# Optimization experiments

Hardware: AMD Instinct MI355X
Metric: run time of the kernel (lower is better)

Reference implementation:

```python
import jax, jax.numpy as jnp
import numpy as np

KS = 3           # kernel size (conv1, conv2, deform conv)
PAD = 1          # k//2 padding for the dense convs and deform zero-padding
DIM = 256
B, H, W = 4, 64, 64
N = KS * KS      # number of sampling points per output pixel


def conv2d(x, w, b=None, pad=PAD, stride=1):
    out = jax.lax.conv_general_dilated(
        x, w, (stride, stride), [(pad, pad), (pad, pad)],
        dimension_numbers=('NCHW', 'OIHW', 'NCHW'))
    if b is not None:
        out = out + b[None, :, None, None]
    return out


def deform_conv(x, p_w, p_b, dw):
    # DeformConv2d (deform-conv-v2 style, modulation=False)
    b, c, h, w = x.shape
    offset = conv2d(x, p_w, p_b, pad=1)                     # (b, 2N, h, w)
    xp = jnp.pad(x, ((0, 0), (0, 0), (PAD, PAD), (PAD, PAD)))
    Hp, Wp = h + 2 * PAD, w + 2 * PAD

    # kernel-relative offsets p_n: rows first, then cols (row-major flatten)
    r = jnp.arange(-(KS - 1) // 2, (KS - 1) // 2 + 1, dtype=x.dtype)
    pnx, pny = jnp.meshgrid(r, r, indexing='ij')
    p_n = jnp.concatenate([pnx.ravel(), pny.ravel()])       # (2N,)

    # base grid p_0 starts at 1 (consistent with zero padding of 1)
    gy, gx = jnp.meshgrid(jnp.arange(1, h + 1, dtype=x.dtype),
                          jnp.arange(1, w + 1, dtype=x.dtype), indexing='ij')
    p0 = jnp.concatenate([jnp.tile(gy[..., None], (1, 1, N)),
                          jnp.tile(gx[..., None], (1, 1, N))], axis=-1)  # (h,w,2N)

    p = jnp.transpose(offset, (0, 2, 3, 1)) + p_n + p0      # (b,h,w,2N)
    px, py = p[..., :N], p[..., N:]
    fx, fy = jnp.floor(px), jnp.floor(py)
    qlx = jnp.clip(fx, 0, Hp - 1)
    qly = jnp.clip(fy, 0, Wp - 1)
    qrx = jnp.clip(fx + 1, 0, Hp - 1)
    qry = jnp.clip(fy + 1, 0, Wp - 1)
    px = jnp.clip(px, 0, Hp - 1)
    py = jnp.clip(py, 0, Wp - 1)

    # bilinear weights
    g_lt = (1 + qlx - px) * (1 + qly - py)
    g_rb = (1 - qrx + px) * (1 - qry + py)
    g_lb = (1 + qlx - px) * (1 - qry + py)
    g_rt = (1 - qrx + px) * (1 + qly - py)

    xf = xp.reshape(b, c, Hp * Wp)

    def gather(qx, qy):
        idx = (qx.astype(jnp.int32) * Wp + qy.astype(jnp.int32)).reshape(b, -1)
        return jax.vmap(lambda xb, ib: xb[:, ib])(xf, idx).reshape(b, c, h, w, N)

    x_off = (g_lt[:, None] * gather(qlx, qly) + g_rb[:, None] * gather(qrx, qry)
           + g_lb[:, None] * gather(qlx, qry) + g_rt[:, None] * gather(qrx, qly))

    # (b,c,h,w,N) -> (b,c,h*ks,w*ks): kernel row expands h, kernel col expands w
    x_off = x_off.reshape(b, c, h, w, KS, KS).transpose(0, 1, 2, 4, 3, 5)
    x_off = x_off.reshape(b, c, h * KS, w * KS)
    return conv2d(x_off, dw, None, pad=0, stride=KS)       # (b, c, h, w)


def setup_inputs() -> dict:
    key = jax.random.key(0)
    ks = jax.random.split(key, 8)
    s = 1.0 / np.sqrt(DIM * KS * KS)
    return {
        'x':   jax.random.normal(ks[0], (B, DIM, H, W), jnp.float32),
        'w1':  jax.random.normal(ks[1], (DIM, DIM, KS, KS), jnp.float32) * s,
        'b1':  jax.random.normal(ks[2], (DIM,), jnp.float32) * 0.01,
        'w2':  jax.random.normal(ks[3], (DIM, DIM, KS, KS), jnp.float32) * s,
        'b2':  jax.random.normal(ks[4], (DIM,), jnp.float32) * 0.01,
        'p_w': jax.random.normal(ks[5], (2 * N, DIM, 3, 3), jnp.float32) * (0.05 * s),
        'p_b': jnp.zeros((2 * N,), jnp.float32),
        'dw':  jax.random.normal(ks[6], (DIM, DIM, KS, KS), jnp.float32) * s,
    }


def reference(x, w1, b1, w2, b2, p_w, p_b, dw):
    res = jax.nn.relu(conv2d(x, w1, b1, pad=PAD))   # conv1 + ReLU
    res = res + x                                   # residual 1
    res = conv2d(res, w2, b2, pad=PAD)              # conv2
    res = deform_conv(res, p_w, p_b, dw)            # deformable conv
    return res + x                                  # residual 2
```

## Files before the change

### kernel.cpp

```cpp
#include <hip/hip_runtime.h>

#define HW 64
#define NB 4
#define CH 256

typedef __attribute__((address_space(1))) const void* gptr_t;
typedef __attribute__((address_space(3))) void* lptr_t;
typedef __attribute__((ext_vector_type(8))) short bf8v;
typedef __attribute__((ext_vector_type(4))) float f32x4;

__device__ __forceinline__ void gll16(const void* g, void* l) {
  __builtin_amdgcn_global_load_lds((gptr_t)g, (lptr_t)l, 16, 0, 0);
}
__device__ __forceinline__ ushort f2b(float f) {
  union { float f; uint u; } v; v.f = f;
  uint r = v.u + 0x7FFF + ((v.u >> 16) & 1);
  return (ushort)(r >> 16);
}
__device__ __forceinline__ uint cvt_pk_bf16(float lo, float hi) {
  uint r;
  asm("v_cvt_pk_bf16_f32 %0, %1, %2" : "=v"(r) : "v"(lo), "v"(hi));
  return r;
}
__device__ __forceinline__ float asf(uint u) {
  union { uint u; float f; } v; v.u = u; return v.f;
}

__device__ __forceinline__ void combine_store(
    const uint4& c0, const uint4& c1, const uint4& c2, const uint4& c3,
    const float4& gw, ushort* dst)
{
  uint o[4];
  const uint* p0 = (const uint*)&c0; const uint* p1 = (const uint*)&c1;
  const uint* p2 = (const uint*)&c2; const uint* p3 = (const uint*)&c3;
  #pragma unroll
  for (int w = 0; w < 4; ++w) {
    const float lo = gw.x * asf(p0[w] << 16) + gw.y * asf(p1[w] << 16)
                   + gw.z * asf(p2[w] << 16) + gw.w * asf(p3[w] << 16);
    const float hi = gw.x * asf(p0[w] & 0xffff0000u) + gw.y * asf(p1[w] & 0xffff0000u)
                   + gw.z * asf(p2[w] & 0xffff0000u) + gw.w * asf(p3[w] & 0xffff0000u);
    o[w] = cvt_pk_bf16(lo, hi);
  }
  uint4 r; r.x = o[0]; r.y = o[1]; r.z = o[2]; r.w = o[3];
  *(uint4*)dst = r;
}

__global__ __launch_bounds__(256) void zero_borders_k(
    ushort* __restrict__ xpad, ushort* __restrict__ res1, ushort* __restrict__ res2)
{
  const int buf = blockIdx.x >> 2, b = blockIdx.x & 3;
  ushort* base = (buf == 0 ? xpad : buf == 1 ? res1 : res2) + (size_t)b * 4356 * 256;
  uint4 z; z.x = 0; z.y = 0; z.z = 0; z.w = 0;
  for (int u = threadIdx.x; u < 260 * 32; u += 256) {
    const int p = u >> 5, k = u & 31;
    int r, cc;
    if (p < 66)       { r = 0;       cc = p; }
    else if (p < 132) { r = 65;      cc = p - 66; }
    else if (p < 196) { r = p - 131; cc = 0; }
    else              { r = p - 195; cc = 65; }
    *(uint4*)&base[((size_t)r * 66 + cc) * 256 + k * 8] = z;
  }
}

__global__ __launch_bounds__(256) void pack_x_k(
    const float* __restrict__ x, ushort* __restrict__ xpad)
{
  __shared__ float tile[64][261];
  const int t = threadIdx.x, b = blockIdx.x >> 6, i = blockIdx.x & 63;
  const int wave = t >> 6, l = t & 63;
  const float* src = x + (size_t)b * CH * 4096 + (size_t)i * 64;
  for (int cc = 0; cc < 64; ++cc) {
    const int c = cc * 4 + wave;
    tile[l][c] = src[(size_t)c * 4096 + l];
  }
  __syncthreads();
  const int c0 = (t & 31) * 8;
  #pragma unroll
  for (int jj = 0; jj < 8; ++jj) {
    const int j = (t >> 5) + jj * 8;
    const float4 v0 = *(const float4*)&tile[j][c0];
    const float4 v1 = *(const float4*)&tile[j][c0 + 4];
    uint4 o;
    o.x = cvt_pk_bf16(v0.x, v0.y);
    o.y = cvt_pk_bf16(v0.z, v0.w);
    o.z = cvt_pk_bf16(v1.x, v1.y);
    o.w = cvt_pk_bf16(v1.z, v1.w);
    *(uint4*)&xpad[((size_t)b * 4356 + (i + 1) * 66 + (j + 1)) * 256 + c0] = o;
  }
}

__global__ __launch_bounds__(256) void pack_w_k(
    const float* __restrict__ w1, const float* __restrict__ w2,
    const float* __restrict__ dw, const float* __restrict__ pw,
    const float* __restrict__ pb,
    ushort* __restrict__ wpk1, ushort* __restrict__ wpk2,
    ushort* __restrict__ dwpk, ushort* __restrict__ wpkO, float* __restrict__ pbias)
{
  const int id = blockIdx.x * 256 + threadIdx.x;
  if (id < 3 * 73728) {
    const int tsel = id / 73728, r = id % 73728;
    const int kc = r & 3, o = (r >> 2) & 255, ct = r >> 10;
    const int cb = ct / 9, tap = ct % 9;
    const float* w = (tsel == 0) ? w1 : (tsel == 1) ? w2 : dw;
    const float* s = w + ((size_t)o * CH + cb * 32 + kc * 8) * 9 + tap;
    ushort* d = ((tsel == 0) ? wpk1 : (tsel == 1) ? wpk2 : dwpk) + (size_t)r * 8;
    #pragma unroll
    for (int j = 0; j < 8; ++j) d[j] = f2b(s[j * 9]);
  } else if (id < 3 * 73728 + 9216) {
    const int r = id - 3 * 73728;
    const int kc = r & 3, o = (r >> 2) & 31, ct = r >> 7;
    const int cb = ct / 9, tap = ct % 9;
    ushort* d = wpkO + (size_t)r * 8;
    if (o < 18) {
      const float* s = pw + ((size_t)o * CH + cb * 32 + kc * 8) * 9 + tap;
      #pragma unroll
      for (int j = 0; j < 8; ++j) d[j] = f2b(s[j * 9]);
    } else {
      #pragma unroll
      for (int j = 0; j < 8; ++j) d[j] = 0;
    }
  }
  if (id < 32) pbias[id] = (id < 18) ? pb[id] : 0.f;
}

template<int OTOT, int OUTMODE>
__global__ __launch_bounds__(256, 4) void conv_mfma(
    const ushort* __restrict__ apad, const ushort* __restrict__ wpk,
    const float* __restrict__ bias, const float* __restrict__ xres,
    void* __restrict__ outp)
{
  __shared__ __align__(16) ushort patch[2][6336];
  const int t = threadIdx.x, wave = t >> 6, l = t & 63;
  const int ot  = (OTOT == 256) ? (blockIdx.x >> 8) : 0;
  const int rem = blockIdx.x & 255;
  const int b = rem >> 6, i = rem & 63;
  const int ln = l & 15, kc8 = (l >> 4) * 8;

  constexpr int FO = (OTOT == 256) ? 1 : 2;
  constexpr int FP = (OTOT == 256) ? 4 : 1;
  const int oS  = (OTOT == 256) ? (ot * 64 + wave * 16) : 0;
  const int pxB = (OTOT == 256) ? 0 : (wave * 16);

  const ushort* rowbase = apad + ((size_t)(b * 66 + i) * 66) * 256;

  f32x4 acc[FO][FP];
  #pragma unroll
  for (int a = 0; a < FO; ++a)
    #pragma unroll
    for (int d = 0; d < FP; ++d) acc[a][d] = (f32x4){0.f, 0.f, 0.f, 0.f};

  #define STAGE(buf, cb)                                                        \
    _Pragma("unroll")                                                           \
    for (int it = 0; it < 4; ++it) {                                            \
      const int e = t + it * 256;                                               \
      if (it < 3 || t < 24) {                                                   \
        const int r = e / 264, u = e - r * 264;                                 \
        const int p = r * 66 + (u >> 2);                                        \
        const int sl = (u & 3) ^ ((p >> 1) & 3);                                \
        const ushort* s = rowbase + (size_t)p * 256 + (cb) * 32 + sl * 8;       \
        gll16(s, (ushort*)&patch[buf][0] + (size_t)e * 8);                      \
      }                                                                         \
    }

  STAGE(0, 0)
  for (int cb = 0; cb < 8; ++cb) {
    __syncthreads();
    bf8v wfr[9][FO];
    #pragma unroll
    for (int tap = 0; tap < 9; ++tap)
      #pragma unroll
      for (int fo = 0; fo < FO; ++fo)
        wfr[tap][fo] = *(const bf8v*)&wpk[((size_t)((cb * 9 + tap) * OTOT) + oS + fo * 16 + ln) * 32 + kc8];
    if (cb < 7) { STAGE((cb + 1) & 1, cb + 1) }
    const ushort* pbuf = &patch[cb & 1][0];
    __builtin_amdgcn_s_setprio(1);
    #pragma unroll
    for (int tap = 0; tap < 9; ++tap) {
      const int ky = tap / 3, kx = tap % 3;
      bf8v pf[FP];
      #pragma unroll
      for (int fp = 0; fp < FP; ++fp) {
        const int px = pxB + fp * 16 + ln;
        const int pix = ky * 66 + px + kx;
        const int sl = (l >> 4) ^ ((pix >> 1) & 3);
        pf[fp] = *(const bf8v*)&pbuf[pix * 32 + sl * 8];
      }
      #pragma unroll
      for (int fo = 0; fo < FO; ++fo)
        #pragma unroll
        for (int fp = 0; fp < FP; ++fp)
          acc[fo][fp] = __builtin_amdgcn_mfma_f32_16x16x32_bf16(wfr[tap][fo], pf[fp], acc[fo][fp], 0, 0, 0);
    }
    __builtin_amdgcn_s_setprio(0);
  }
  #undef STAGE

  #pragma unroll
  for (int fo = 0; fo < FO; ++fo) {
    #pragma unroll
    for (int fp = 0; fp < FP; ++fp) {
      const f32x4 a = acc[fo][fp];
      const int o = oS + fo * 16 + (l >> 4) * 4;
      const int j = pxB + fp * 16 + ln;
      const float4 bv = *(const float4*)&bias[o];
      float v0 = a[0] + bv.x, v1 = a[1] + bv.y, v2 = a[2] + bv.z, v3 = a[3] + bv.w;
      if (OUTMODE == 0) {
        const size_t xb = (((size_t)b * CH + o) * HW + i) * HW + j;
        v0 = fmaxf(v0, 0.f) + xres[xb];
        v1 = fmaxf(v1, 0.f) + xres[xb + 4096];
        v2 = fmaxf(v2, 0.f) + xres[xb + 8192];
        v3 = fmaxf(v3, 0.f) + xres[xb + 12288];
      }
      if (OUTMODE == 2) {
        float* op = (float*)outp + ((size_t)b * 4096 + i * 64 + j) * 32 + o;
        float4 r; r.x = v0; r.y = v1; r.z = v2; r.w = v3;
        *(float4*)op = r;
      } else {
        ushort* op = (ushort*)outp + ((size_t)b * 4356 + (i + 1) * 66 + (j + 1)) * 256 + o;
        ushort4 s; s.x = f2b(v0); s.y = f2b(v1); s.z = f2b(v2); s.w = f2b(v3);
        *(ushort4*)op = s;
      }
    }
  }
}

__global__ __launch_bounds__(512) void deform_mfma(
    const ushort* __restrict__ res2pad, const float* __restrict__ offs,
    const ushort* __restrict__ dwpk, const float* __restrict__ x,
    float* __restrict__ out)
{
  __shared__ __align__(16) ushort samp[18432];
  __shared__ __align__(16) int    tblI[576 * 4];
  __shared__ __align__(16) float  tblW[576 * 4];

  const int t = threadIdx.x, wave = t >> 6, l = t & 63;
  const int ohalf = blockIdx.x >> 8;
  const int idx = blockIdx.x & 255;
  const int blk = (idx & 7) * 32 + (idx >> 3);
  const int b = blk >> 6, i = blk & 63;
  const int ln = l & 15, kc8 = (l >> 4) * 8;
  const int oS = ohalf * 128 + wave * 16;

  #pragma unroll
  for (int k2 = 0; k2 < 2; ++k2) {
    const int e = t + k2 * 512;
    if (e < 576) {
      const int n = e >> 6, j = e & 63;
      const int ki = n / 3, kj = n % 3;
      const float offr = offs[((size_t)(b * 64 + i) * 64 + j) * 32 + n];
      const float offc = offs[((size_t)(b * 64 + i) * 64 + j) * 32 + 9 + n];
      const float prow = offr + (float)(ki - 1) + (float)(i + 1);
      const float pcol = offc + (float)(kj - 1) + (float)(j + 1);
      const float fx = floorf(prow), fy = floorf(pcol);
      const float qlx = fminf(fmaxf(fx, 0.f), 65.f);
      const float qly = fminf(fmaxf(fy, 0.f), 65.f);
      const float qrx = fminf(fmaxf(fx + 1.f, 0.f), 65.f);
      const float qry = fminf(fmaxf(fy + 1.f, 0.f), 65.f);
      const float pr  = fminf(fmaxf(prow, 0.f), 65.f);
      const float pc  = fminf(fmaxf(pcol, 0.f), 65.f);
      tblI[e * 4 + 0] = ((int)qlx * 66 + (int)qly) * 512;
      tblI[e * 4 + 1] = ((int)qrx * 66 + (int)qry) * 512;
      tblI[e * 4 + 2] = ((int)qlx * 66 + (int)qry) * 512;
      tblI[e * 4 + 3] = ((int)qrx * 66 + (int)qly) * 512;
      tblW[e * 4 + 0] = (1.f + qlx - pr) * (1.f + qly - pc);
      tblW[e * 4 + 1] = (1.f - qrx + pr) * (1.f - qry + pc);
      tblW[e * 4 + 2] = (1.f + qlx - pr) * (1.f - qry + pc);
      tblW[e * 4 + 3] = (1.f - qrx + pr) * (1.f + qly - pc);
    }
  }

  f32x4 acc[4];
  #pragma unroll
  for (int a = 0; a < 4; ++a) acc[a] = (f32x4){0.f, 0.f, 0.f, 0.f};

  const char* res2b = (const char*)(res2pad + (size_t)b * 4356 * 256);

  #define SAMPLE_CB(cb_)                                                        \
    _Pragma("unroll")                                                           \
    for (int k = 0; k < 5; ++k) {                                               \
      if (k < 4 || t < 256) {                                                   \
        const int u = t + k * 512;                                              \
        const int e = u >> 2, i16 = u & 3;                                      \
        const int4 iv = *(const int4*)&tblI[e * 4];                             \
        const float4 gw = *(const float4*)&tblW[e * 4];                         \
        const char* gb = res2b + (cb_) * 64 + i16 * 16;                         \
        const uint4 c0 = *(const uint4*)(gb + iv.x);                            \
        const uint4 c1 = *(const uint4*)(gb + iv.y);                            \
        const uint4 c2 = *(const uint4*)(gb + iv.z);                            \
        const uint4 c3 = *(const uint4*)(gb + iv.w);                            \
        const int sl = i16 ^ ((e >> 1) & 3);                                    \
        combine_store(c0, c1, c2, c3, gw, &samp[(size_t)e * 32 + sl * 8]);      \
      }                                                                         \
    }

  __syncthreads();
  SAMPLE_CB(0)
  __syncthreads();

  const int rsl = ((l >> 4) ^ ((ln >> 1) & 3)) * 8;

  for (int cb = 0; cb < 8; ++cb) {
    const ushort* wbase = dwpk + (size_t)(cb * 9) * 256 * 32;

    bf8v bfrA[3], bfrB[3];
    #pragma unroll
    for (int q = 0; q < 3; ++q)
      bfrA[q] = *(const bf8v*)&wbase[((size_t)q * 256 + oS + ln) * 32 + kc8];

    #pragma unroll
    for (int ch = 0; ch < 3; ++ch) {
      if (ch < 2) {
        #pragma unroll
        for (int q = 0; q < 3; ++q)
          bfrB[q] = *(const bf8v*)&wbase[((size_t)((ch + 1) * 3 + q) * 256 + oS + ln) * 32 + kc8];
      }
      __builtin_amdgcn_s_setprio(1);
      #pragma unroll
      for (int q = 0; q < 3; ++q) {
        const int tap = ch * 3 + q;
        #pragma unroll
        for (int fp = 0; fp < 4; ++fp) {
          const bf8v af = *(const bf8v*)&samp[(tap * 64 + fp * 16 + ln) * 32 + rsl];
          acc[fp] = __builtin_amdgcn_mfma_f32_16x16x32_bf16(af, bfrA[q], acc[fp], 0, 0, 0);
        }
      }
      __builtin_amdgcn_s_setprio(0);
      #pragma unroll
      for (int q = 0; q < 3; ++q) bfrA[q] = bfrB[q];
    }

    __syncthreads();
    if (cb < 7) {
      SAMPLE_CB(cb + 1)
      __syncthreads();
    }
  }
  #undef SAMPLE_CB

  #pragma unroll
  for (int fp = 0; fp < 4; ++fp) {
    const f32x4 a = acc[fp];
    const int o = oS + ln;
    const int j0 = fp * 16 + (l >> 4) * 4;
    const size_t base = (((size_t)b * CH + o) * HW + i) * HW + j0;
    const float4 xv = *(const float4*)&x[base];
    float4 r; r.x = a[0] + xv.x; r.y = a[1] + xv.y; r.z = a[2] + xv.z; r.w = a[3] + xv.w;
    *(float4*)&out[base] = r;
  }
}

extern "C" void kernel_launch(void* const* d_in, const int* in_sizes, int n_in,
                              void* d_out, int out_size, void* d_ws, size_t ws_size,
                              hipStream_t stream) {
  (void)in_sizes; (void)n_in; (void)out_size; (void)ws_size;
  const float* x  = (const float*)d_in[0];
  const float* w1 = (const float*)d_in[1];
  const float* b1 = (const float*)d_in[2];
  const float* w2 = (const float*)d_in[3];
  const float* b2 = (const float*)d_in[4];
  const float* pw = (const float*)d_in[5];
  const float* pb = (const float*)d_in[6];
  const float* dw = (const float*)d_in[7];
  float* out = (float*)d_out;

  char* w = (char*)d_ws;
  size_t off = 0;
  auto carve = [&](size_t bytes) { char* p = w + off; off += (bytes + 255) & ~(size_t)255; return p; };
  ushort* xpad  = (ushort*)carve(8929280);
  ushort* res1  = (ushort*)carve(8929280);
  ushort* res2  = (ushort*)carve(8929280);
  ushort* wpk1  = (ushort*)carve(1179648);
  ushort* wpk2  = (ushort*)carve(1179648);
  ushort* wpkO  = (ushort*)carve(147456);
  ushort* dwpk  = (ushort*)carve(1179648);
  float*  pbias = (float*) carve(256);
  float*  offs  = (float*) carve(2097152);

  zero_borders_k<<<12, 256, 0, stream>>>(xpad, res1, res2);
  pack_w_k<<<900, 256, 0, stream>>>(w1, w2, dw, pw, pb, wpk1, wpk2, dwpk, wpkO, pbias);
  pack_x_k<<<256, 256, 0, stream>>>(x, xpad);
  conv_mfma<256, 0><<<1024, 256, 0, stream>>>(xpad, wpk1, b1, x, res1);
  conv_mfma<256, 1><<<1024, 256, 0, stream>>>(res1, wpk2, b2, nullptr, res2);
  conv_mfma<32, 2><<<256, 256, 0, stream>>>(res2, wpkO, pbias, nullptr, offs);
  deform_mfma<<<NB * HW * 2, 512, 0, stream>>>(res2, offs, dwpk, x, out);
}
```

Before: 145.6 us.

## Split deform conv blocks by column half instead of output-channel half

The deform kernel now splits each output row into two 32-column halves across blocks, with 16 waves covering all 256 output channels, instead of splitting output channels in half. Each block therefore samples only its own 32 columns, so the bilinear gather and offset-table work is no longer duplicated across the two channel-half blocks, and shared memory per block is halved. The cost is 1024-thread blocks with fewer MFMA tiles per wave, which may lower latency hiding or occupancy per wave.

```diff
diff --git a/kernel.cpp b/kernel.cpp
--- a/kernel.cpp
+++ b/kernel.cpp
@@ -224,62 +224,59 @@
   }
 }
 
-__global__ __launch_bounds__(512) void deform_mfma(
+__global__ __launch_bounds__(1024) void deform_mfma(
     const ushort* __restrict__ res2pad, const float* __restrict__ offs,
     const ushort* __restrict__ dwpk, const float* __restrict__ x,
     float* __restrict__ out)
 {
-  __shared__ __align__(16) ushort samp[18432];
-  __shared__ __align__(16) int    tblI[576 * 4];
-  __shared__ __align__(16) float  tblW[576 * 4];
+  __shared__ __align__(16) ushort samp[9216];
+  __shared__ __align__(16) int    tblI[288 * 4];
+  __shared__ __align__(16) float  tblW[288 * 4];
 
   const int t = threadIdx.x, wave = t >> 6, l = t & 63;
-  const int ohalf = blockIdx.x >> 8;
+  const int jh = blockIdx.x >> 8;
   const int idx = blockIdx.x & 255;
   const int blk = (idx & 7) * 32 + (idx >> 3);
   const int b = blk >> 6, i = blk & 63;
   const int ln = l & 15, kc8 = (l >> 4) * 8;
-  const int oS = ohalf * 128 + wave * 16;
-
-  #pragma unroll
-  for (int k2 = 0; k2 < 2; ++k2) {
-    const int e = t + k2 * 512;
-    if (e < 576) {
-      const int n = e >> 6, j = e & 63;
-      const int ki = n / 3, kj = n % 3;
-      const float offr = offs[((size_t)(b * 64 + i) * 64 + j) * 32 + n];
-      const float offc = offs[((size_t)(b * 64 + i) * 64 + j) * 32 + 9 + n];
-      const float prow = offr + (float)(ki - 1) + (float)(i + 1);
-      const float pcol = offc + (float)(kj - 1) + (float)(j + 1);
-      const float fx = floorf(prow), fy = floorf(pcol);
-      const float qlx = fminf(fmaxf(fx, 0.f), 65.f);
-      const float qly = fminf(fmaxf(fy, 0.f), 65.f);
-      const float qrx = fminf(fmaxf(fx + 1.f, 0.f), 65.f);
-      const float qry = fminf(fmaxf(fy + 1.f, 0.f), 65.f);
-      const float pr  = fminf(fmaxf(prow, 0.f), 65.f);
-      const float pc  = fminf(fmaxf(pcol, 0.f), 65.f);
-      tblI[e * 4 + 0] = ((int)qlx * 66 + (int)qly) * 512;
-      tblI[e * 4 + 1] = ((int)qrx * 66 + (int)qry) * 512;
-      tblI[e * 4 + 2] = ((int)qlx * 66 + (int)qry) * 512;
-      tblI[e * 4 + 3] = ((int)qrx * 66 + (int)qly) * 512;
-      tblW[e * 4 + 0] = (1.f + qlx - pr) * (1.f + qly - pc);
-      tblW[e * 4 + 1] = (1.f - qrx + pr) * (1.f - qry + pc);
-      tblW[e * 4 + 2] = (1.f + qlx - pr) * (1.f - qry + pc);
-      tblW[e * 4 + 3] = (1.f - qrx + pr) * (1.f + qly - pc);
-    }
-  }
-
-  f32x4 acc[4];
-  #pragma unroll
-  for (int a = 0; a < 4; ++a) acc[a] = (f32x4){0.f, 0.f, 0.f, 0.f};
+  const int oS = wave * 16;
+
+  if (t < 288) {
+    const int n = t >> 5, jj = t & 31;
+    const int j = jh * 32 + jj;
+    const int ki = n / 3, kj = n % 3;
+    const float offr = offs[((size_t)(b * 64 + i) * 64 + j) * 32 + n];
+    const float offc = offs[((size_t)(b * 64 + i) * 64 + j) * 32 + 9 + n];
+    const float prow = offr + (float)(ki - 1) + (float)(i + 1);
+    const float pcol = offc + (float)(kj - 1) + (float)(j + 1);
+    const float fx = floorf(prow), fy = floorf(pcol);
+    const float qlx = fminf(fmaxf(fx, 0.f), 65.f);
+    const float qly = fminf(fmaxf(fy, 0.f), 65.f);
+    const float qrx = fminf(fmaxf(fx + 1.f, 0.f), 65.f);
+    const float qry = fminf(fmaxf(fy + 1.f, 0.f), 65.f);
+    const float pr  = fminf(fmaxf(prow, 0.f), 65.f);
+    const float pc  = fminf(fmaxf(pcol, 0.f), 65.f);
+    tblI[t * 4 + 0] = ((int)qlx * 66 + (int)qly) * 512;
+    tblI[t * 4 + 1] = ((int)qrx * 66 + (int)qry) * 512;
+    tblI[t * 4 + 2] = ((int)qlx * 66 + (int)qry) * 512;
+    tblI[t * 4 + 3] = ((int)qrx * 66 + (int)qly) * 512;
+    tblW[t * 4 + 0] = (1.f + qlx - pr) * (1.f + qly - pc);
+    tblW[t * 4 + 1] = (1.f - qrx + pr) * (1.f - qry + pc);
+    tblW[t * 4 + 2] = (1.f + qlx - pr) * (1.f - qry + pc);
+    tblW[t * 4 + 3] = (1.f - qrx + pr) * (1.f + qly - pc);
+  }
+
+  f32x4 acc[2];
+  acc[0] = (f32x4){0.f, 0.f, 0.f, 0.f};
+  acc[1] = (f32x4){0.f, 0.f, 0.f, 0.f};
 
   const char* res2b = (const char*)(res2pad + (size_t)b * 4356 * 256);
 
   #define SAMPLE_CB(cb_)                                                        \
     _Pragma("unroll")                                                           \
-    for (int k = 0; k < 5; ++k) {                                               \
-      if (k < 4 || t < 256) {                                                   \
-        const int u = t + k * 512;                                              \
+    for (int k = 0; k < 2; ++k) {                                               \
+      if (k == 0 || t < 128) {                                                  \
+        const int u = t + k * 1024;                                             \
         const int e = u >> 2, i16 = u & 3;                                      \
         const int4 iv = *(const int4*)&tblI[e * 4];                             \
         const float4 gw = *(const float4*)&tblW[e * 4];                         \
@@ -319,8 +316,8 @@
       for (int q = 0; q < 3; ++q) {
         const int tap = ch * 3 + q;
         #pragma unroll
-        for (int fp = 0; fp < 4; ++fp) {
-          const bf8v af = *(const bf8v*)&samp[(tap * 64 + fp * 16 + ln) * 32 + rsl];
+        for (int fp = 0; fp < 2; ++fp) {
+          const bf8v af = *(const bf8v*)&samp[(tap * 32 + fp * 16 + ln) * 32 + rsl];
           acc[fp] = __builtin_amdgcn_mfma_f32_16x16x32_bf16(af, bfrA[q], acc[fp], 0, 0, 0);
         }
       }
@@ -338,10 +335,10 @@
   #undef SAMPLE_CB
 
   #pragma unroll
-  for (int fp = 0; fp < 4; ++fp) {
+  for (int fp = 0; fp < 2; ++fp) {
     const f32x4 a = acc[fp];
     const int o = oS + ln;
-    const int j0 = fp * 16 + (l >> 4) * 4;
+    const int j0 = jh * 32 + fp * 16 + (l >> 4) * 4;
     const size_t base = (((size_t)b * CH + o) * HW + i) * HW + j0;
     const float4 xv = *(const float4*)&x[base];
     float4 r; r.x = a[0] + xv.x; r.y = a[1] + xv.y; r.z = a[2] + xv.z; r.w = a[3] + xv.w;
@@ -382,5 +379,5 @@
   conv_mfma<256, 0><<<1024, 256, 0, stream>>>(xpad, wpk1, b1, x, res1);
   conv_mfma<256, 1><<<1024, 256, 0, stream>>>(res1, wpk2, b2, nullptr, res2);
   conv_mfma<32, 2><<<256, 256, 0, stream>>>(res2, wpkO, pbias, nullptr, offs);
-  deform_mfma<<<NB * HW * 2, 512, 0, stream>>>(res2, offs, dwpk, x, out);
-}
+  deform_mfma<<<NB * HW * 2, 1024, 0, stream>>>(res2, offs, dwpk, x, out);
+}
```

Result: slower. 149.2 us (+2.5%).

## Double output channels per block in convs and deform, double-buffer deform samples

Applied to the files above, without the earlier changes.

The dense conv kernels now compute 32 output channels per wave (128 per block) instead of 64 per block, halving the grid and reusing each staged input patch across twice as many channels. Weight fragments are loaded in three chunks of three taps rather than all nine at once, to limit register pressure. The deform kernel now covers all 256 output channels per block, so the bilinear sampling, which was previously done twice for the two channel halves, runs once. Its sample buffer is double-buffered so the next channel block's gather overlaps the MFMAs, with one sync per iteration. The cost is more accumulators per wave, lower occupancy bounds, and only 256 deform blocks and 512 conv blocks, which may underfill the GPU.

```diff
diff --git a/kernel.cpp b/kernel.cpp
--- a/kernel.cpp
+++ b/kernel.cpp
@@ -124,7 +124,7 @@
 }
 
 template<int OTOT, int OUTMODE>
-__global__ __launch_bounds__(256, 4) void conv_mfma(
+__global__ __launch_bounds__(256, 2) void conv_mfma(
     const ushort* __restrict__ apad, const ushort* __restrict__ wpk,
     const float* __restrict__ bias, const float* __restrict__ xres,
     void* __restrict__ outp)
@@ -136,9 +136,9 @@
   const int b = rem >> 6, i = rem & 63;
   const int ln = l & 15, kc8 = (l >> 4) * 8;
 
-  constexpr int FO = (OTOT == 256) ? 1 : 2;
+  constexpr int FO = 2;
   constexpr int FP = (OTOT == 256) ? 4 : 1;
-  const int oS  = (OTOT == 256) ? (ot * 64 + wave * 16) : 0;
+  const int oS  = (OTOT == 256) ? (ot * 128 + wave * 32) : 0;
   const int pxB = (OTOT == 256) ? 0 : (wave * 16);
 
   const ushort* rowbase = apad + ((size_t)(b * 66 + i) * 66) * 256;
@@ -165,33 +165,36 @@
   STAGE(0, 0)
   for (int cb = 0; cb < 8; ++cb) {
     __syncthreads();
-    bf8v wfr[9][FO];
-    #pragma unroll
-    for (int tap = 0; tap < 9; ++tap)
-      #pragma unroll
-      for (int fo = 0; fo < FO; ++fo)
-        wfr[tap][fo] = *(const bf8v*)&wpk[((size_t)((cb * 9 + tap) * OTOT) + oS + fo * 16 + ln) * 32 + kc8];
-    if (cb < 7) { STAGE((cb + 1) & 1, cb + 1) }
     const ushort* pbuf = &patch[cb & 1][0];
-    __builtin_amdgcn_s_setprio(1);
-    #pragma unroll
-    for (int tap = 0; tap < 9; ++tap) {
-      const int ky = tap / 3, kx = tap % 3;
-      bf8v pf[FP];
-      #pragma unroll
-      for (int fp = 0; fp < FP; ++fp) {
-        const int px = pxB + fp * 16 + ln;
-        const int pix = ky * 66 + px + kx;
-        const int sl = (l >> 4) ^ ((pix >> 1) & 3);
-        pf[fp] = *(const bf8v*)&pbuf[pix * 32 + sl * 8];
-      }
-      #pragma unroll
-      for (int fo = 0; fo < FO; ++fo)
+    #pragma unroll
+    for (int ch = 0; ch < 3; ++ch) {
+      bf8v wfr[3][FO];
+      #pragma unroll
+      for (int q = 0; q < 3; ++q) {
+        const int tap = ch * 3 + q;
         #pragma unroll
-        for (int fp = 0; fp < FP; ++fp)
-          acc[fo][fp] = __builtin_amdgcn_mfma_f32_16x16x32_bf16(wfr[tap][fo], pf[fp], acc[fo][fp], 0, 0, 0);
-    }
-    __builtin_amdgcn_s_setprio(0);
+        for (int fo = 0; fo < FO; ++fo)
+          wfr[q][fo] = *(const bf8v*)&wpk[((size_t)((cb * 9 + tap) * OTOT) + oS + fo * 16 + ln) * 32 + kc8];
+      }
+      if (ch == 2 && cb < 7) { STAGE((cb + 1) & 1, cb + 1) }
+      __builtin_amdgcn_s_setprio(1);
+      #pragma unroll
+      for (int q = 0; q < 3; ++q) {
+        const int tap = ch * 3 + q;
+        const int ky = tap / 3, kx = tap % 3;
+        #pragma unroll
+        for (int fp = 0; fp < FP; ++fp) {
+          const int px = pxB + fp * 16 + ln;
+          const int pix = ky * 66 + px + kx;
+          const int sl = (l >> 4) ^ ((pix >> 1) & 3);
+          const bf8v pf = *(const bf8v*)&pbuf[pix * 32 + sl * 8];
+          #pragma unroll
+          for (int fo = 0; fo < FO; ++fo)
+            acc[fo][fp] = __builtin_amdgcn_mfma_f32_16x16x32_bf16(wfr[q][fo], pf, acc[fo][fp], 0, 0, 0);
+        }
+      }
+      __builtin_amdgcn_s_setprio(0);
+    }
   }
   #undef STAGE
 
@@ -224,22 +227,20 @@
   }
 }
 
-__global__ __launch_bounds__(512) void deform_mfma(
+__global__ __launch_bounds__(512, 2) void deform_mfma(
     const ushort* __restrict__ res2pad, const float* __restrict__ offs,
     const ushort* __restrict__ dwpk, const float* __restrict__ x,
     float* __restrict__ out)
 {
-  __shared__ __align__(16) ushort samp[18432];
+  __shared__ __align__(16) ushort samp[2][18432];
   __shared__ __align__(16) int    tblI[576 * 4];
   __shared__ __align__(16) float  tblW[576 * 4];
 
   const int t = threadIdx.x, wave = t >> 6, l = t & 63;
-  const int ohalf = blockIdx.x >> 8;
-  const int idx = blockIdx.x & 255;
-  const int blk = (idx & 7) * 32 + (idx >> 3);
+  const int blk = (blockIdx.x & 7) * 32 + (blockIdx.x >> 3);
   const int b = blk >> 6, i = blk & 63;
   const int ln = l & 15, kc8 = (l >> 4) * 8;
-  const int oS = ohalf * 128 + wave * 16;
+  const int oS = wave * 32;
 
   #pragma unroll
   for (int k2 = 0; k2 < 2; ++k2) {
@@ -269,13 +270,15 @@
     }
   }
 
-  f32x4 acc[4];
-  #pragma unroll
-  for (int a = 0; a < 4; ++a) acc[a] = (f32x4){0.f, 0.f, 0.f, 0.f};
+  f32x4 acc[2][4];
+  #pragma unroll
+  for (int a = 0; a < 2; ++a)
+    #pragma unroll
+    for (int d = 0; d < 4; ++d) acc[a][d] = (f32x4){0.f, 0.f, 0.f, 0.f};
 
   const char* res2b = (const char*)(res2pad + (size_t)b * 4356 * 256);
 
-  #define SAMPLE_CB(cb_)                                                        \
+  #define SAMPLE_CB(cb_, buf_)                                                  \
     _Pragma("unroll")                                                           \
     for (int k = 0; k < 5; ++k) {                                               \
       if (k < 4 || t < 256) {                                                   \
@@ -289,63 +292,60 @@
         const uint4 c2 = *(const uint4*)(gb + iv.z);                            \
         const uint4 c3 = *(const uint4*)(gb + iv.w);                            \
         const int sl = i16 ^ ((e >> 1) & 3);                                    \
-        combine_store(c0, c1, c2, c3, gw, &samp[(size_t)e * 32 + sl * 8]);      \
+        combine_store(c0, c1, c2, c3, gw, &samp[buf_][(size_t)e * 32 + sl * 8]);\
       }                                                                         \
     }
 
   __syncthreads();
-  SAMPLE_CB(0)
+  SAMPLE_CB(0, 0)
   __syncthreads();
 
   const int rsl = ((l >> 4) ^ ((ln >> 1) & 3)) * 8;
 
   for (int cb = 0; cb < 8; ++cb) {
+    const ushort* sb = &samp[cb & 1][0];
     const ushort* wbase = dwpk + (size_t)(cb * 9) * 256 * 32;
 
-    bf8v bfrA[3], bfrB[3];
-    #pragma unroll
-    for (int q = 0; q < 3; ++q)
-      bfrA[q] = *(const bf8v*)&wbase[((size_t)q * 256 + oS + ln) * 32 + kc8];
-
     #pragma unroll
     for (int ch = 0; ch < 3; ++ch) {
-      if (ch < 2) {
+      bf8v bfr[3][2];
+      #pragma unroll
+      for (int q = 0; q < 3; ++q)
         #pragma unroll
-        for (int q = 0; q < 3; ++q)
-          bfrB[q] = *(const bf8v*)&wbase[((size_t)((ch + 1) * 3 + q) * 256 + oS + ln) * 32 + kc8];
-      }
+        for (int fo = 0; fo < 2; ++fo)
+          bfr[q][fo] = *(const bf8v*)&wbase[((size_t)((ch * 3 + q) * 256) + oS + fo * 16 + ln) * 32 + kc8];
       __builtin_amdgcn_s_setprio(1);
       #pragma unroll
       for (int q = 0; q < 3; ++q) {
         const int tap = ch * 3 + q;
         #pragma unroll
         for (int fp = 0; fp < 4; ++fp) {
-          const bf8v af = *(const bf8v*)&samp[(tap * 64 + fp * 16 + ln) * 32 + rsl];
-          acc[fp] = __builtin_amdgcn_mfma_f32_16x16x32_bf16(af, bfrA[q], acc[fp], 0, 0, 0);
+          const bf8v af = *(const bf8v*)&sb[(tap * 64 + fp * 16 + ln) * 32 + rsl];
+          #pragma unroll
+          for (int fo = 0; fo < 2; ++fo)
+            acc[fo][fp] = __builtin_amdgcn_mfma_f32_16x16x32_bf16(af, bfr[q][fo], acc[fo][fp], 0, 0, 0);
         }
       }
       __builtin_amdgcn_s_setprio(0);
-      #pragma unroll
-      for (int q = 0; q < 3; ++q) bfrA[q] = bfrB[q];
-    }
-
+    }
+
+    if (cb < 7) { SAMPLE_CB(cb + 1, (cb + 1) & 1) }
     __syncthreads();
-    if (cb < 7) {
-      SAMPLE_CB(cb + 1)
-      __syncthreads();
-    }
   }
   #undef SAMPLE_CB
 
   #pragma unroll
-  for (int fp = 0; fp < 4; ++fp) {
-    const f32x4 a = acc[fp];
-    const int o = oS + ln;
-    const int j0 = fp * 16 + (l >> 4) * 4;
-    const size_t base = (((size_t)b * CH + o) * HW + i) * HW + j0;
-    const float4 xv = *(const float4*)&x[base];
-    float4 r; r.x = a[0] + xv.x; r.y = a[1] + xv.y; r.z = a[2] + xv.z; r.w = a[3] + xv.w;
-    *(float4*)&out[base] = r;
+  for (int fo = 0; fo < 2; ++fo) {
+    #pragma unroll
+    for (int fp = 0; fp < 4; ++fp) {
+      const f32x4 a = acc[fo][fp];
+      const int o = oS + fo * 16 + ln;
+      const int j0 = fp * 16 + (l >> 4) * 4;
+      const size_t base = (((size_t)b * CH + o) * HW + i) * HW + j0;
+      const float4 xv = *(const float4*)&x[base];
+      float4 r; r.x = a[0] + xv.x; r.y = a[1] + xv.y; r.z = a[2] + xv.z; r.w = a[3] + xv.w;
+      *(float4*)&out[base] = r;
+    }
   }
 }
 
@@ -379,8 +379,8 @@
   zero_borders_k<<<12, 256, 0, stream>>>(xpad, res1, res2);
   pack_w_k<<<900, 256, 0, stream>>>(w1, w2, dw, pw, pb, wpk1, wpk2, dwpk, wpkO, pbias);
   pack_x_k<<<256, 256, 0, stream>>>(x, xpad);
-  conv_mfma<256, 0><<<1024, 256, 0, stream>>>(xpad, wpk1, b1, x, res1);
-  conv_mfma<256, 1><<<1024, 256, 0, stream>>>(res1, wpk2, b2, nullptr, res2);
+  conv_mfma<256, 0><<<512, 256, 0, stream>>>(xpad, wpk1, b1, x, res1);
+  conv_mfma<256, 1><<<512, 256, 0, stream>>>(res1, wpk2, b2, nullptr, res2);
   conv_mfma<32, 2><<<256, 256, 0, stream>>>(res2, wpkO, pbias, nullptr, offs);
-  deform_mfma<<<NB * HW * 2, 512, 0, stream>>>(res2, offs, dwpk, x, out);
-}
+  deform_mfma<<<NB * HW, 512, 0, stream>>>(res2, offs, dwpk, x, out);
+}
```

After: 129.3 us. -11.2%, faster.
